# Performance work log

Measured on AMD Instinct MI355X. Metric: run time of the kernel, lower is better.

The kernel has to match this reference:

```python
import jax, jax.numpy as jnp
import numpy as np

B, C, N, K, OUT = 4, 64, 16384, 20, 64
S = max(1, int(np.ceil(K * 0.5)))  # sample_k = 10
EPS = 1e-5
SLOPE = 0.2


def setup_inputs() -> dict:
    key = jax.random.key(0)
    k1, k2, k3, k4, k5 = jax.random.split(key, 5)
    x = jax.random.normal(k1, (B, C, N), dtype=jnp.float32)
    common_idx_flat = jax.random.randint(k2, (B * N * K,), 0, B * N)
    rand_scores = jax.random.uniform(k3, (B, N, K), dtype=jnp.float32)
    dw_weight = jax.random.normal(k4, (2 * C,), dtype=jnp.float32) * 0.5
    pw_weight = jax.random.normal(k5, (OUT, 2 * C), dtype=jnp.float32) * (1.0 / np.sqrt(2 * C))
    bn_gamma = jnp.ones((2 * C,), dtype=jnp.float32)
    bn_beta = jnp.zeros((2 * C,), dtype=jnp.float32)
    return {"x": x, "common_idx_flat": common_idx_flat, "rand_scores": rand_scores,
            "dw_weight": dw_weight, "pw_weight": pw_weight,
            "bn_gamma": bn_gamma, "bn_beta": bn_beta}


def reference(x, common_idx_flat, rand_scores, dw_weight, pw_weight, bn_gamma, bn_beta):
    b, c, n = x.shape
    # --- sample S of the K precomputed neighbors via random-score topk ---
    idx_mat = common_idx_flat.reshape(b, n, K)               # flat indices into (B*N)
    _, pos = jax.lax.top_k(rand_scores, S)                   # (B,N,S) positions in [0,K)
    sampled = jnp.take_along_axis(idx_mat, pos, axis=2)      # (B,N,S)
    # --- gather edge features: [neighbor - central, central] ---
    xt = jnp.transpose(x, (0, 2, 1)).reshape(b * n, c)       # (B*N, C)
    neigh = xt[sampled.reshape(-1)].reshape(b, n, S, c)      # (B,N,S,C)
    central = xt.reshape(b, n, 1, c)
    edge = jnp.concatenate([neigh - central,
                            jnp.broadcast_to(central, (b, n, S, c))], axis=-1)  # (B,N,S,2C)
    # --- depthwise 1x1 conv (per-channel scale), BN (training stats), LeakyReLU ---
    dw = edge * dw_weight
    mean = dw.mean(axis=(0, 1, 2))
    var = dw.var(axis=(0, 1, 2))                              # biased, as torch BN
    dwn = (dw - mean) * jax.lax.rsqrt(var + EPS) * bn_gamma + bn_beta
    act = jnp.where(dwn > 0, dwn, SLOPE * dwn)
    # --- pointwise 1x1 conv, then max over neighbors ---
    out = jnp.einsum('bnsc,oc->bons', act, pw_weight)         # (B,OUT,N,S)
    return out.max(axis=-1)                                   # (B,OUT,N)
```

## Files before the change

kernel.cpp:

```cpp
#include <hip/hip_runtime.h>
#include <hip/hip_bf16.h>

#define B_   4
#define C_   64
#define N_   16384
#define K_   20
#define S_   10
#define OUT_ 64
#define CH_  128
#define ROWS_ (B_ * N_)
#define RST_ 16

typedef __attribute__((ext_vector_type(4))) float  f32x4;
typedef __attribute__((ext_vector_type(8))) __bf16 bf16x8;
typedef __attribute__((ext_vector_type(4))) __bf16 bf16x4;
typedef __attribute__((ext_vector_type(4))) unsigned short u16x4;

__device__ inline float bf2f(unsigned short u) {
  union { unsigned int i; float f; } x; x.i = ((unsigned int)u) << 16; return x.f;
}

__global__ __launch_bounds__(256) void k_prep(
    const float* __restrict__ x, __bf16* __restrict__ xt,
    const float* __restrict__ scores, const int* __restrict__ idxmat,
    int* __restrict__ sampled, float* __restrict__ statsR,
    const float* __restrict__ pw, __bf16* __restrict__ pwb) {
  const int bid = blockIdx.x;
  const int t   = threadIdx.x;
  if (bid < 4096) {
    __shared__ float tile[32][33];
    const int nt = bid & 511, ct = (bid >> 9) & 1, b = bid >> 10;
    const int n0 = nt * 32, c0 = ct * 32;
    const int tx = t & 31, ty = t >> 5;
#pragma unroll
    for (int k = 0; k < 32; k += 8)
      tile[ty + k][tx] = x[((size_t)(b * C_ + c0 + ty + k)) * N_ + n0 + tx];
    __syncthreads();
    const int nl = t >> 3;
    const int cb = (t & 7) * 4;
    bf16x4 p;
#pragma unroll
    for (int i = 0; i < 4; ++i) p[i] = (__bf16)tile[cb + i][nl];
    *(bf16x4*)&xt[((size_t)(b * N_ + n0 + nl)) * C_ + c0 + cb] = p;
  } else if (bid < 4352) {
    if (bid == 4096) {
#pragma unroll
      for (int i = 0; i < RST_; ++i) statsR[i * 256 + t] = 0.f;
    }
    const int j = (bid - 4096) * 256 + t;
    const float* sc = scores + (size_t)j * K_;
    const int*   id = idxmat + (size_t)j * K_;
    float sv[K_]; int iv[K_];
#pragma unroll
    for (int k = 0; k < K_; ++k) { sv[k] = sc[k]; iv[k] = id[k]; }
    int* outp = sampled + (size_t)j * S_;
#pragma unroll
    for (int k = 0; k < K_; ++k) {
      const float sk = sv[k];
      int rank = 0;
#pragma unroll
      for (int m = 0; m < K_; ++m)
        rank += ((sv[m] > sk) || (sv[m] == sk && m < k)) ? 1 : 0;
      if (rank < S_) outp[rank] = iv[k];
    }
  } else {
    const int o  = 16 * (t >> 6) + (t & 15);
    const int kb = 8 * ((t >> 4) & 3);
    const float* src = pw + (size_t)o * CH_;
    __bf16* dst = pwb + t * 32;
#pragma unroll
    for (int ts = 0; ts < 2; ++ts)
#pragma unroll
      for (int i = 0; i < 8; ++i) {
        dst[ts * 8 + i]      = (__bf16)src[32 * ts + kb + i];
        dst[16 + ts * 8 + i] = (__bf16)src[C_ + 32 * ts + kb + i];
      }
  }
}

__global__ __launch_bounds__(256, 4) void k_stats(const __bf16* __restrict__ xt,
                                                  const int* __restrict__ sampled,
                                                  float* __restrict__ statsR) {
  const int t    = threadIdx.x;
  const int lane = t & 63;
  const int w    = t >> 6;
  const int r    = t >> 4;
  const int q    = t & 15;
  const int j0   = blockIdx.x * 32;
  const int jA   = j0 + r;
  const int jB   = j0 + 16 + r;

  int ia[S_], ib[S_];
  const int* spA = sampled + (size_t)jA * S_;
  const int* spB = sampled + (size_t)jB * S_;
#pragma unroll
  for (int s = 0; s < S_; ++s) { ia[s] = spA[s]; ib[s] = spB[s]; }

  u16x4 cA = *(const u16x4*)&xt[jA * C_ + 4 * q];
  u16x4 cB = *(const u16x4*)&xt[jB * C_ + 4 * q];

  u16x4 vA[S_], vB[S_];
#pragma unroll
  for (int s = 0; s < S_; ++s) {
    vA[s] = *(const u16x4*)&xt[ia[s] * C_ + 4 * q];
    vB[s] = *(const u16x4*)&xt[ib[s] * C_ + 4 * q];
  }
  __builtin_amdgcn_sched_barrier(0);

  f32x4 sd = {0,0,0,0}, qd = {0,0,0,0}, sc = {0,0,0,0}, qc = {0,0,0,0};
  float cenA[4], cenB[4];
#pragma unroll
  for (int i = 0; i < 4; ++i) {
    cenA[i] = bf2f(cA[i]); cenB[i] = bf2f(cB[i]);
    sc[i] += cenA[i] + cenB[i];
    qc[i] += cenA[i] * cenA[i] + cenB[i] * cenB[i];
  }
#pragma unroll
  for (int s = 0; s < S_; ++s) {
#pragma unroll
    for (int i = 0; i < 4; ++i) {
      const float dA = bf2f(vA[s][i]) - cenA[i];
      const float dB = bf2f(vB[s][i]) - cenB[i];
      sd[i] += dA + dB;
      qd[i] += dA * dA + dB * dB;
    }
  }

#pragma unroll
  for (int i = 0; i < 4; ++i) {
    sd[i] += __shfl_xor(sd[i], 16); sd[i] += __shfl_xor(sd[i], 32);
    qd[i] += __shfl_xor(qd[i], 16); qd[i] += __shfl_xor(qd[i], 32);
    sc[i] += __shfl_xor(sc[i], 16); sc[i] += __shfl_xor(sc[i], 32);
    qc[i] += __shfl_xor(qc[i], 16); qc[i] += __shfl_xor(qc[i], 32);
  }

  __shared__ float sred[4][4][64];
  if (lane < 16) {
    *(f32x4*)&sred[0][w][4 * q] = sd;
    *(f32x4*)&sred[1][w][4 * q] = qd;
    *(f32x4*)&sred[2][w][4 * q] = sc;
    *(f32x4*)&sred[3][w][4 * q] = qc;
  }
  __syncthreads();
  if (t < 64) {
    float* dst = statsR + (blockIdx.x & (RST_ - 1)) * 256;
#pragma unroll
    for (int k = 0; k < 4; ++k) {
      const float v = sred[k][0][t] + sred[k][1][t] + sred[k][2][t] + sred[k][3][t];
      atomicAdd(&dst[k * 64 + t], v);
    }
  }
}

__global__ void k_fold(const float* __restrict__ statsR, const float* __restrict__ dww,
                       const float* __restrict__ gamma, const float* __restrict__ beta,
                       float* __restrict__ AB) {
  __shared__ float sstat[256];
  const int t = threadIdx.x;
  float sv = 0.f;
#pragma unroll
  for (int rr = 0; rr < RST_; ++rr) sv += statsR[rr * 256 + t];
  sstat[t] = sv;
  __syncthreads();
  if (t < CH_) {
    float mean_e, var_e;
    if (t < C_) {
      const float cnt = (float)ROWS_ * (float)S_;
      const float su = sstat[t], sq = sstat[64 + t];
      mean_e = su / cnt; var_e = sq / cnt - mean_e * mean_e;
    } else {
      const float cnt = (float)ROWS_;
      const float su = sstat[128 + (t - C_)], sq = sstat[192 + (t - C_)];
      mean_e = su / cnt; var_e = sq / cnt - mean_e * mean_e;
    }
    const float wg = dww[t], g = gamma[t];
    const float inv = rsqrtf(wg * wg * var_e + 1e-5f);
    AB[t]       = wg * g * inv;
    AB[CH_ + t] = beta[t] - wg * mean_e * inv * g;
  }
}

__global__ __launch_bounds__(256, 4) void k_main(
    const __bf16* __restrict__ xt, const int* __restrict__ sampled,
    const float* __restrict__ AB, const __bf16* __restrict__ pwb,
    float* __restrict__ out) {
  __shared__ __bf16 dact[160 * 64];
  __shared__ __bf16 cact[16 * 64];
  float* ost = (float*)dact;

  const int t    = threadIdx.x;
  const int lane = t & 63;
  const int w    = t >> 6;
  const int j0   = blockIdx.x * 16;
  const int b    = j0 / N_;
  const int n0   = j0 % N_;
  const int r    = t >> 4;
  const int q    = t & 15;

  int nb[S_];
  const int* sp = sampled + (size_t)(j0 + r) * S_;
#pragma unroll
  for (int s = 0; s < S_; ++s) nb[s] = sp[s];
  u16x4 cu = *(const u16x4*)&xt[(j0 + r) * C_ + 4 * q];
  u16x4 vu[S_];
#pragma unroll
  for (int s = 0; s < S_; ++s)
    vu[s] = *(const u16x4*)&xt[nb[s] * C_ + 4 * q];

  const f32x4 a_d = *(const f32x4*)&AB[4 * q];
  const f32x4 a_c = *(const f32x4*)&AB[C_ + 4 * q];
  const f32x4 b_d = *(const f32x4*)&AB[CH_ + 4 * q];
  const f32x4 b_c = *(const f32x4*)&AB[CH_ + C_ + 4 * q];

  bf16x8 bfd[2], bfc[2];
  {
    const bf16x8* fp = (const bf16x8*)(pwb + t * 32);
    bfd[0] = fp[0]; bfd[1] = fp[1]; bfc[0] = fp[2]; bfc[1] = fp[3];
  }
  __builtin_amdgcn_sched_barrier(0);

  float cen[4];
  {
    bf16x4 p;
#pragma unroll
    for (int i = 0; i < 4; ++i) {
      cen[i] = bf2f(cu[i]);
      const float tt = a_c[i] * cen[i] + b_c[i];
      p[i] = (__bf16)fmaxf(tt, 0.2f * tt);
    }
    const int byt = r * 128 + ((8 * q) ^ ((r & 7) << 4));
    *(bf16x4*)((char*)cact + byt) = p;
  }

#pragma unroll
  for (int s = 0; s < S_; ++s) {
    bf16x4 p;
#pragma unroll
    for (int i = 0; i < 4; ++i) {
      const float d  = bf2f(vu[s][i]) - cen[i];
      const float tt = a_d[i] * d + b_d[i];
      p[i] = (__bf16)fmaxf(tt, 0.2f * tt);
    }
    const int row = s * 16 + r;
    const int byt = row * 128 + ((8 * q) ^ ((r & 7) << 4));
    *(bf16x4*)((char*)dact + byt) = p;
  }

  __syncthreads();

  const int arow  = lane & 15;
  const int akoff = 16 * (lane >> 4);
  const int swz   = (arow & 7) << 4;

  f32x4 cacc = {0.f, 0.f, 0.f, 0.f};
#pragma unroll
  for (int ts = 0; ts < 2; ++ts) {
    bf16x8 a = *(bf16x8*)((char*)cact + arow * 128 + ((64 * ts + akoff) ^ swz));
    cacc = __builtin_amdgcn_mfma_f32_16x16x32_bf16(a, bfc[ts], cacc, 0, 0, 0);
  }

  f32x4 rmax;
  rmax[0] = rmax[1] = rmax[2] = rmax[3] = -__builtin_inff();
#pragma unroll
  for (int s = 0; s < S_; ++s) {
    f32x4 acc = {0.f, 0.f, 0.f, 0.f};
#pragma unroll
    for (int ts = 0; ts < 2; ++ts) {
      bf16x8 a = *(bf16x8*)((char*)dact + (s * 16 + arow) * 128 + ((64 * ts + akoff) ^ swz));
      acc = __builtin_amdgcn_mfma_f32_16x16x32_bf16(a, bfd[ts], acc, 0, 0, 0);
    }
#pragma unroll
    for (int i = 0; i < 4; ++i) rmax[i] = fmaxf(rmax[i], acc[i]);
  }

  __syncthreads();
  {
    const int ol = lane & 15;
    const int rb = 4 * (lane >> 4);
#pragma unroll
    for (int i = 0; i < 4; ++i) ost[(rb + i) * 68 + 16 * w + ol] = rmax[i] + cacc[i];
  }
  __syncthreads();
  {
    const int o  = t >> 2;
    const int sg = t & 3;
    f32x4 v;
#pragma unroll
    for (int i = 0; i < 4; ++i) v[i] = ost[(sg * 4 + i) * 68 + o];
    *(f32x4*)&out[((size_t)(b * OUT_ + o)) * N_ + n0 + sg * 4] = v;
  }
}

extern "C" void kernel_launch(void* const* d_in, const int* in_sizes, int n_in,
                              void* d_out, int out_size, void* d_ws, size_t ws_size,
                              hipStream_t stream) {
  const float* x      = (const float*)d_in[0];
  const int*   cif    = (const int*)  d_in[1];
  const float* scores = (const float*)d_in[2];
  const float* dww    = (const float*)d_in[3];
  const float* pw     = (const float*)d_in[4];
  const float* gamma  = (const float*)d_in[5];
  const float* beta   = (const float*)d_in[6];
  float* out = (float*)d_out;

  char* ws = (char*)d_ws;
  __bf16* xt      = (__bf16*)(ws);
  int*    sampled = (int*)   (ws + 8388608);
  float*  statsR  = (float*) (ws + 8388608 + 2621440);
  float*  AB      = (float*) (ws + 8388608 + 2621440 + 16384);
  __bf16* pwb     = (__bf16*)(ws + 8388608 + 2621440 + 16384 + 1024);

  k_prep<<<4096 + 256 + 1, 256, 0, stream>>>(x, xt, scores, cif, sampled, statsR, pw, pwb);
  k_stats<<<ROWS_ / 32, 256, 0, stream>>>(xt, sampled, statsR);
  k_fold<<<1, 256, 0, stream>>>(statsR, dww, gamma, beta, AB);
  k_main<<<ROWS_ / 16, 256, 0, stream>>>(xt, sampled, AB, pwb, out);
}
```

Baseline: 57.48 us.

## Prescale features in a separate pass and make k_main LDS-free per wave

The one-block fold kernel becomes a grid-wide scale kernel. Each block recomputes the BN affine terms, then writes a per-channel scaled copy of the features (xd) and the precomputed central-branch activation (actc). k_main now gives each wave 16 points and all 64 outputs, building MFMA A-operands straight from gathered registers with no LDS staging or block barriers, and writes output directly. This removes the per-point affine math and the LDS round-trips from the gather kernel. In exchange it adds an extra full pass that writes two bf16 feature copies, and rounding a_d*x to bf16 before the subtraction changes precision slightly.

```diff
diff --git a/kernel.cpp b/kernel.cpp
--- a/kernel.cpp
+++ b/kernel.cpp
@@ -15,6 +15,7 @@
 typedef __attribute__((ext_vector_type(8))) __bf16 bf16x8;
 typedef __attribute__((ext_vector_type(4))) __bf16 bf16x4;
 typedef __attribute__((ext_vector_type(4))) unsigned short u16x4;
+typedef __attribute__((ext_vector_type(8))) unsigned short u16x8;
 
 __device__ inline float bf2f(unsigned short u) {
   union { unsigned int i; float f; } x; x.i = ((unsigned int)u) << 16; return x.f;
@@ -24,7 +25,7 @@
     const float* __restrict__ x, __bf16* __restrict__ xt,
     const float* __restrict__ scores, const int* __restrict__ idxmat,
     int* __restrict__ sampled, float* __restrict__ statsR,
-    const float* __restrict__ pw, __bf16* __restrict__ pwb) {
+    const float* __restrict__ pw, __bf16* __restrict__ pwb2) {
   const int bid = blockIdx.x;
   const int t   = threadIdx.x;
   if (bid < 4096) {
@@ -64,17 +65,17 @@
       if (rank < S_) outp[rank] = iv[k];
     }
   } else {
-    const int o  = 16 * (t >> 6) + (t & 15);
-    const int kb = 8 * ((t >> 4) & 3);
-    const float* src = pw + (size_t)o * CH_;
-    __bf16* dst = pwb + t * 32;
-#pragma unroll
-    for (int ts = 0; ts < 2; ++ts)
-#pragma unroll
-      for (int i = 0; i < 8; ++i) {
-        dst[ts * 8 + i]      = (__bf16)src[32 * ts + kb + i];
-        dst[16 + ts * 8 + i] = (__bf16)src[C_ + 32 * ts + kb + i];
-      }
+#pragma unroll
+    for (int pass = 0; pass < 2; ++pass) {
+      const int e   = t + pass * 256;
+      const int col = e & 15, ks = (e >> 4) & 3, ts = (e >> 6) & 1, og = (e >> 7) & 3;
+      const float* src = pw + (size_t)(16 * og + col) * CH_ + 32 * ts + 8 * ks;
+      bf16x8 dv, cv;
+#pragma unroll
+      for (int i = 0; i < 8; ++i) { dv[i] = (__bf16)src[i]; cv[i] = (__bf16)src[C_ + i]; }
+      *(bf16x8*)&pwb2[e * 8]        = dv;
+      *(bf16x8*)&pwb2[4096 + e * 8] = cv;
+    }
   }
 }
 
@@ -152,10 +153,13 @@
   }
 }
 
-__global__ void k_fold(const float* __restrict__ statsR, const float* __restrict__ dww,
-                       const float* __restrict__ gamma, const float* __restrict__ beta,
-                       float* __restrict__ AB) {
+__global__ __launch_bounds__(256) void k_scale(
+    const float* __restrict__ statsR, const float* __restrict__ dww,
+    const float* __restrict__ gamma, const float* __restrict__ beta,
+    const __bf16* __restrict__ xt, __bf16* __restrict__ xd,
+    __bf16* __restrict__ actc, float* __restrict__ AB) {
   __shared__ float sstat[256];
+  __shared__ float abf[256];
   const int t = threadIdx.x;
   float sv = 0.f;
 #pragma unroll
@@ -166,128 +170,127 @@
     float mean_e, var_e;
     if (t < C_) {
       const float cnt = (float)ROWS_ * (float)S_;
-      const float su = sstat[t], sq = sstat[64 + t];
-      mean_e = su / cnt; var_e = sq / cnt - mean_e * mean_e;
+      mean_e = sstat[t] / cnt; var_e = sstat[64 + t] / cnt - mean_e * mean_e;
     } else {
       const float cnt = (float)ROWS_;
-      const float su = sstat[128 + (t - C_)], sq = sstat[192 + (t - C_)];
-      mean_e = su / cnt; var_e = sq / cnt - mean_e * mean_e;
+      mean_e = sstat[128 + (t - C_)] / cnt; var_e = sstat[192 + (t - C_)] / cnt - mean_e * mean_e;
     }
     const float wg = dww[t], g = gamma[t];
     const float inv = rsqrtf(wg * wg * var_e + 1e-5f);
-    AB[t]       = wg * g * inv;
-    AB[CH_ + t] = beta[t] - wg * mean_e * inv * g;
-  }
-}
-
-__global__ __launch_bounds__(256, 4) void k_main(
-    const __bf16* __restrict__ xt, const int* __restrict__ sampled,
-    const float* __restrict__ AB, const __bf16* __restrict__ pwb,
-    float* __restrict__ out) {
-  __shared__ __bf16 dact[160 * 64];
-  __shared__ __bf16 cact[16 * 64];
-  float* ost = (float*)dact;
-
-  const int t    = threadIdx.x;
-  const int lane = t & 63;
-  const int w    = t >> 6;
-  const int j0   = blockIdx.x * 16;
-  const int b    = j0 / N_;
-  const int n0   = j0 % N_;
-  const int r    = t >> 4;
-  const int q    = t & 15;
+    abf[t]       = wg * g * inv;
+    abf[CH_ + t] = beta[t] - wg * mean_e * inv * g;
+  }
+  __syncthreads();
+  if (blockIdx.x == 0) AB[t] = abf[t];
+
+  const int g   = blockIdx.x * 256 + t;
+  const int row = g >> 3;
+  const int c8  = (g & 7) * 8;
+  u16x8 xv = *(const u16x8*)&xt[(size_t)row * C_ + c8];
+  bf16x8 xdv, acv;
+#pragma unroll
+  for (int i = 0; i < 8; ++i) {
+    const int c = c8 + i;
+    const float f = bf2f(xv[i]);
+    xdv[i] = (__bf16)(abf[c] * f);
+    const float tc = abf[C_ + c] * f + abf[CH_ + C_ + c];
+    acv[i] = (__bf16)fmaxf(tc, 0.2f * tc);
+  }
+  *(bf16x8*)&xd[(size_t)row * C_ + c8]   = xdv;
+  *(bf16x8*)&actc[(size_t)row * C_ + c8] = acv;
+}
+
+__global__ __launch_bounds__(256, 3) void k_main(
+    const __bf16* __restrict__ xd, const __bf16* __restrict__ actc,
+    const int* __restrict__ sampled, const float* __restrict__ AB,
+    const __bf16* __restrict__ pwb2, float* __restrict__ out) {
+  const int t   = threadIdx.x;
+  const int l   = t & 63;
+  const int w   = t >> 6;
+  const int j0  = blockIdx.x * 64 + w * 16;
+  const int b   = j0 / N_;
+  const int n0  = j0 % N_;
+  const int col = l & 15;
+  const int ks  = l >> 4;
+  const int jr  = j0 + col;
+  const int cb  = 8 * ks;
 
   int nb[S_];
-  const int* sp = sampled + (size_t)(j0 + r) * S_;
+  const int* sp = sampled + (size_t)jr * S_;
 #pragma unroll
   for (int s = 0; s < S_; ++s) nb[s] = sp[s];
-  u16x4 cu = *(const u16x4*)&xt[(j0 + r) * C_ + 4 * q];
-  u16x4 vu[S_];
-#pragma unroll
-  for (int s = 0; s < S_; ++s)
-    vu[s] = *(const u16x4*)&xt[nb[s] * C_ + 4 * q];
-
-  const f32x4 a_d = *(const f32x4*)&AB[4 * q];
-  const f32x4 a_c = *(const f32x4*)&AB[C_ + 4 * q];
-  const f32x4 b_d = *(const f32x4*)&AB[CH_ + 4 * q];
-  const f32x4 b_c = *(const f32x4*)&AB[CH_ + C_ + 4 * q];
-
-  bf16x8 bfd[2], bfc[2];
-  {
-    const bf16x8* fp = (const bf16x8*)(pwb + t * 32);
-    bfd[0] = fp[0]; bfd[1] = fp[1]; bfc[0] = fp[2]; bfc[1] = fp[3];
-  }
+
+  u16x8 vd[S_][2];
+#pragma unroll
+  for (int s = 0; s < S_; ++s) {
+    const __bf16* p = xd + (size_t)nb[s] * C_ + cb;
+    vd[s][0] = *(const u16x8*)p;
+    vd[s][1] = *(const u16x8*)(p + 32);
+  }
+  u16x8 cd0 = *(const u16x8*)(xd + (size_t)jr * C_ + cb);
+  u16x8 cd1 = *(const u16x8*)(xd + (size_t)jr * C_ + cb + 32);
+
+  f32x4 b0a = *(const f32x4*)&AB[CH_ + cb];
+  f32x4 b0b = *(const f32x4*)&AB[CH_ + cb + 4];
+  f32x4 b1a = *(const f32x4*)&AB[CH_ + 32 + cb];
+  f32x4 b1b = *(const f32x4*)&AB[CH_ + 32 + cb + 4];
+
+  bf16x8 bfd[2][4];
+#pragma unroll
+  for (int og = 0; og < 4; ++og)
+#pragma unroll
+    for (int ts = 0; ts < 2; ++ts)
+      bfd[ts][og] = *(const bf16x8*)&pwb2[(((og * 2 + ts) * 4 + ks) * 16 + col) * 8];
   __builtin_amdgcn_sched_barrier(0);
 
-  float cen[4];
-  {
-    bf16x4 p;
-#pragma unroll
-    for (int i = 0; i < 4; ++i) {
-      cen[i] = bf2f(cu[i]);
-      const float tt = a_c[i] * cen[i] + b_c[i];
-      p[i] = (__bf16)fmaxf(tt, 0.2f * tt);
-    }
-    const int byt = r * 128 + ((8 * q) ^ ((r & 7) << 4));
-    *(bf16x4*)((char*)cact + byt) = p;
-  }
+  float cc[16];
+#pragma unroll
+  for (int i = 0; i < 4; ++i) {
+    cc[i]      = bf2f(cd0[i])     - b0a[i];
+    cc[4 + i]  = bf2f(cd0[4 + i]) - b0b[i];
+    cc[8 + i]  = bf2f(cd1[i])     - b1a[i];
+    cc[12 + i] = bf2f(cd1[4 + i]) - b1b[i];
+  }
+
+  f32x4 rmax[4];
+#pragma unroll
+  for (int og = 0; og < 4; ++og)
+    rmax[og][0] = rmax[og][1] = rmax[og][2] = rmax[og][3] = -__builtin_inff();
 
 #pragma unroll
   for (int s = 0; s < S_; ++s) {
-    bf16x4 p;
-#pragma unroll
-    for (int i = 0; i < 4; ++i) {
-      const float d  = bf2f(vu[s][i]) - cen[i];
-      const float tt = a_d[i] * d + b_d[i];
-      p[i] = (__bf16)fmaxf(tt, 0.2f * tt);
-    }
-    const int row = s * 16 + r;
-    const int byt = row * 128 + ((8 * q) ^ ((r & 7) << 4));
-    *(bf16x4*)((char*)dact + byt) = p;
-  }
-
-  __syncthreads();
-
-  const int arow  = lane & 15;
-  const int akoff = 16 * (lane >> 4);
-  const int swz   = (arow & 7) << 4;
-
-  f32x4 cacc = {0.f, 0.f, 0.f, 0.f};
-#pragma unroll
-  for (int ts = 0; ts < 2; ++ts) {
-    bf16x8 a = *(bf16x8*)((char*)cact + arow * 128 + ((64 * ts + akoff) ^ swz));
-    cacc = __builtin_amdgcn_mfma_f32_16x16x32_bf16(a, bfc[ts], cacc, 0, 0, 0);
-  }
-
-  f32x4 rmax;
-  rmax[0] = rmax[1] = rmax[2] = rmax[3] = -__builtin_inff();
-#pragma unroll
-  for (int s = 0; s < S_; ++s) {
-    f32x4 acc = {0.f, 0.f, 0.f, 0.f};
-#pragma unroll
-    for (int ts = 0; ts < 2; ++ts) {
-      bf16x8 a = *(bf16x8*)((char*)dact + (s * 16 + arow) * 128 + ((64 * ts + akoff) ^ swz));
-      acc = __builtin_amdgcn_mfma_f32_16x16x32_bf16(a, bfd[ts], acc, 0, 0, 0);
-    }
-#pragma unroll
-    for (int i = 0; i < 4; ++i) rmax[i] = fmaxf(rmax[i], acc[i]);
-  }
-
-  __syncthreads();
-  {
-    const int ol = lane & 15;
-    const int rb = 4 * (lane >> 4);
-#pragma unroll
-    for (int i = 0; i < 4; ++i) ost[(rb + i) * 68 + 16 * w + ol] = rmax[i] + cacc[i];
-  }
-  __syncthreads();
-  {
-    const int o  = t >> 2;
-    const int sg = t & 3;
+    bf16x8 a0, a1;
+#pragma unroll
+    for (int i = 0; i < 8; ++i) {
+      const float f0 = bf2f(vd[s][0][i]) - cc[i];
+      a0[i] = (__bf16)fmaxf(f0, 0.2f * f0);
+      const float f1 = bf2f(vd[s][1][i]) - cc[8 + i];
+      a1[i] = (__bf16)fmaxf(f1, 0.2f * f1);
+    }
+#pragma unroll
+    for (int og = 0; og < 4; ++og) {
+      f32x4 acc = {0.f, 0.f, 0.f, 0.f};
+      acc = __builtin_amdgcn_mfma_f32_16x16x32_bf16(a0, bfd[0][og], acc, 0, 0, 0);
+      acc = __builtin_amdgcn_mfma_f32_16x16x32_bf16(a1, bfd[1][og], acc, 0, 0, 0);
+#pragma unroll
+      for (int i = 0; i < 4; ++i) rmax[og][i] = fmaxf(rmax[og][i], acc[i]);
+    }
+  }
+  __builtin_amdgcn_sched_barrier(0);
+
+  bf16x8 ac0 = *(const bf16x8*)(actc + (size_t)jr * C_ + cb);
+  bf16x8 ac1 = *(const bf16x8*)(actc + (size_t)jr * C_ + cb + 32);
+#pragma unroll
+  for (int og = 0; og < 4; ++og) {
+    bf16x8 c0 = *(const bf16x8*)&pwb2[4096 + (((og * 2 + 0) * 4 + ks) * 16 + col) * 8];
+    bf16x8 c1 = *(const bf16x8*)&pwb2[4096 + (((og * 2 + 1) * 4 + ks) * 16 + col) * 8];
+    f32x4 cacc = {0.f, 0.f, 0.f, 0.f};
+    cacc = __builtin_amdgcn_mfma_f32_16x16x32_bf16(ac0, c0, cacc, 0, 0, 0);
+    cacc = __builtin_amdgcn_mfma_f32_16x16x32_bf16(ac1, c1, cacc, 0, 0, 0);
     f32x4 v;
 #pragma unroll
-    for (int i = 0; i < 4; ++i) v[i] = ost[(sg * 4 + i) * 68 + o];
-    *(f32x4*)&out[((size_t)(b * OUT_ + o)) * N_ + n0 + sg * 4] = v;
+    for (int i = 0; i < 4; ++i) v[i] = rmax[og][i] + cacc[i];
+    *(f32x4*)&out[(size_t)(b * OUT_ + 16 * og + col) * N_ + n0 + 4 * ks] = v;
   }
 }
 
@@ -306,12 +309,14 @@
   char* ws = (char*)d_ws;
   __bf16* xt      = (__bf16*)(ws);
   int*    sampled = (int*)   (ws + 8388608);
-  float*  statsR  = (float*) (ws + 8388608 + 2621440);
-  float*  AB      = (float*) (ws + 8388608 + 2621440 + 16384);
-  __bf16* pwb     = (__bf16*)(ws + 8388608 + 2621440 + 16384 + 1024);
-
-  k_prep<<<4096 + 256 + 1, 256, 0, stream>>>(x, xt, scores, cif, sampled, statsR, pw, pwb);
+  float*  statsR  = (float*) (ws + 11010048);
+  float*  AB      = (float*) (ws + 11026432);
+  __bf16* pwb2    = (__bf16*)(ws + 11027456);
+  __bf16* xd      = (__bf16*)(ws + 11043840);
+  __bf16* actc    = (__bf16*)(ws + 19432448);
+
+  k_prep<<<4096 + 256 + 1, 256, 0, stream>>>(x, xt, scores, cif, sampled, statsR, pw, pwb2);
   k_stats<<<ROWS_ / 32, 256, 0, stream>>>(xt, sampled, statsR);
-  k_fold<<<1, 256, 0, stream>>>(statsR, dww, gamma, beta, AB);
-  k_main<<<ROWS_ / 16, 256, 0, stream>>>(xt, sampled, AB, pwb, out);
-}
+  k_scale<<<ROWS_ * C_ / 8 / 256, 256, 0, stream>>>(statsR, dww, gamma, beta, xt, xd, actc, AB);
+  k_main<<<ROWS_ / 64, 256, 0, stream>>>(xd, actc, sampled, AB, pwb2, out);
+}
```

Result: slower. 63.13 us (+9.8%).
